# Optimization experiments

Hardware: AMD Instinct MI355X
Metric: run time of the kernel (lower is better)

The kernel has to match this reference:

```python
import jax, jax.numpy as jnp
import numpy as np

VOCAB = 64
EMBED = 256
HIDDEN = 1024
BATCH = 256
SEQLEN = 512


def setup_inputs() -> dict:
    key = jax.random.key(0)
    ks = jax.random.split(key, 5)
    return {
        "x": jax.random.randint(ks[0], (BATCH, SEQLEN), 0, VOCAB),
        "embedding": jax.random.normal(ks[1], (VOCAB, EMBED), dtype=jnp.float32),
        "W_ih": jax.random.normal(ks[2], (EMBED, HIDDEN), dtype=jnp.float32) * 0.01,
        "W_hh": jax.random.normal(ks[3], (HIDDEN, HIDDEN), dtype=jnp.float32) * 0.01,
        "b_h": jnp.zeros((HIDDEN,), dtype=jnp.float32),
        "W_ho": jax.random.normal(ks[4], (HIDDEN, VOCAB), dtype=jnp.float32) * 0.01,
        "b_o": jnp.zeros((VOCAB,), dtype=jnp.float32),
    }


def reference(x, embedding, W_ih, W_hh, b_h, W_ho, b_o):
    # x: [B, L] int indices
    b, l = x.shape
    x_embed = embedding[x]                 # [B, L, E]
    # Precompute the input projection for all timesteps at once: [L, B, H]
    x_proj = jnp.einsum('ble,eh->lbh', x_embed, W_ih) + b_h
    h0 = jnp.zeros((b, W_hh.shape[0]), dtype=x_embed.dtype)

    def step(h_prev, xp_t):
        h_t = jnp.tanh(xp_t + h_prev @ W_hh)   # [B, H]
        return h_t, h_t

    final_hidden, outputs = jax.lax.scan(step, h0, x_proj)  # outputs: [L, B, H]
    outputs = outputs.transpose(1, 0, 2)                    # [B, L, H]
    logits = outputs @ W_ho + b_o                           # [B, L, V]
    return logits, final_hidden
```

## Files before the change

### kernel.cpp

```cpp
#include <hip/hip_runtime.h>
#include <stdint.h>


#define BATCH 256
#define SEQ   512
#define HID   1024
#define VOC   64
#define EMB   256
#define FINAL_OFF (BATCH * SEQ * VOC)
#define RING_SLOTS 32
#define BH (BATCH * HID)
#define CNT_STRIDE 8448

typedef __attribute__((ext_vector_type(8))) short short8;
typedef __attribute__((ext_vector_type(4))) float f32x4;
typedef unsigned long long u64;

__device__ inline unsigned short f2bf(float f) {
  union { float f; unsigned u; } v; v.f = f;
  unsigned u = v.u;
  return (unsigned short)((u + 0x7FFFu + ((u >> 16) & 1u)) >> 16);
}

__device__ __forceinline__ float ftanh(float v) {
  float e = __expf(2.0f * v);
  return fmaf(-2.0f, __builtin_amdgcn_rcpf(e + 1.0f), 1.0f);
}

__device__ inline u64 cload64(const unsigned short* p) {
  return __hip_atomic_load((const u64*)p, __ATOMIC_RELAXED,
                           __HIP_MEMORY_SCOPE_AGENT);
}
__device__ inline void cstore32(unsigned short* p, unsigned v) {
  __hip_atomic_store((unsigned*)p, v, __ATOMIC_RELAXED,
                     __HIP_MEMORY_SCOPE_AGENT);
}

__global__ __launch_bounds__(256) void k_prep(const float* __restrict__ emb,
                                              const float* __restrict__ Wih,
                                              const float* __restrict__ bh,
                                              float* __restrict__ proj) {
  __shared__ float es[EMB];
  const int v = blockIdx.x >> 2;
  const int p = blockIdx.x & 3;
  const int tid = threadIdx.x;
  es[tid] = emb[v * EMB + tid];
  __syncthreads();
  const int h = p * 256 + tid;
  float acc = bh[h];
  for (int e = 0; e < EMB; ++e) acc += es[e] * Wih[e * HID + h];
  proj[v * HID + h] = acc;
}

__global__ __launch_bounds__(256) void k_prep2(const float* __restrict__ Who,
                                               unsigned short* __restrict__ wof) {
  const int e = blockIdx.x * 256 + threadIdx.x;
  const int l15 = e & 15, vt = (e >> 4) & 3, qq = (e >> 6) & 3, kb = e >> 8;
  #pragma unroll
  for (int j = 0; j < 8; ++j)
    wof[e * 8 + j] = f2bf(Who[(kb * 32 + qq * 8 + j) * VOC + vt * 16 + l15]);
}

__global__ __launch_bounds__(256, 1) void k_rnn(
    const int* __restrict__ x, const float* __restrict__ Whh,
    const float* __restrict__ proj, const unsigned short* __restrict__ wof,
    const float* __restrict__ bo, unsigned short* __restrict__ ring,
    float* __restrict__ out, float* __restrict__ final_out,
    unsigned int* __restrict__ cnt) {
  extern __shared__ char smem[];
  unsigned short* w_lds = (unsigned short*)smem;
  char*           h_lds = smem;
  float*          p_lds = (float*)(smem + 33024);
  int*            xs_t  = (int*)(smem + 49664);

  const int tid = threadIdx.x, bid = blockIdx.x;
  const int gi = bid & 15, gj = bid >> 4;
  const int row0 = gi * 16;
  const int lane = tid & 63, wv = tid >> 6;
  const int l15 = lane & 15, q = lane >> 4;

  for (int it = 0; it < 256; ++it) {
    int u = it * 256 + tid;
    int k = u >> 6, n = u & 63;
    int kb = k >> 5, qq = (k >> 3) & 3, j8 = k & 7;
    w_lds[(size_t)kb * 2048 + qq * 512 + n * 8 + j8] =
        f2bf(Whh[k * HID + gj * 64 + n]);
  }
  __syncthreads();

  short8 bfr[32];
  {
    const char* bbase = (const char*)w_lds + q * 1024 + (wv * 16 + l15) * 16;
    #pragma unroll
    for (int kb = 0; kb < 32; ++kb)
      bfr[kb] = *(const short8*)(bbase + (size_t)kb * 4096);
  }
  __syncthreads();

  for (int it = 0; it < 16; ++it) {
    int u = it * 256 + tid;
    int v = u >> 6, c = u & 63;
    p_lds[v * 65 + c] = proj[(size_t)v * HID + gj * 64 + c];
  }
  for (int it = 0; it < 32; ++it) {
    int u = it * 256 + tid;
    int tt = u >> 4, r = u & 15;
    xs_t[tt * 16 + r] = x[(size_t)(row0 + r) * SEQ + tt];
  }
  __syncthreads();

  unsigned int* cnt_i = (unsigned int*)((char*)cnt + gi * CNT_STRIDE);

  const int hcol = gj * 64 + wv * 16 + l15;
  const int pcol = wv * 16 + l15;
  const char* abase = h_lds + l15 * 2064 + q * 16;
  const float bias = bo[wv * 16 + l15];
  const char* wofb = (const char*)wof + ((q * 4 + wv) * 16 + l15) * 16;

  for (int t = 0; t < SEQ; ++t) {
    f32x4 a0 = {0.f, 0.f, 0.f, 0.f}, a1 = {0.f, 0.f, 0.f, 0.f};
    f32x4 a2 = {0.f, 0.f, 0.f, 0.f}, a3 = {0.f, 0.f, 0.f, 0.f};
    if (t > 0) {
      #pragma unroll
      for (int kb = 0; kb < 32; kb += 4) {
        short8 af0 = *(const short8*)(abase + (kb + 0) * 64);
        a0 = __builtin_amdgcn_mfma_f32_16x16x32_bf16(af0, bfr[kb + 0], a0, 0, 0, 0);
        short8 af1 = *(const short8*)(abase + (kb + 1) * 64);
        a1 = __builtin_amdgcn_mfma_f32_16x16x32_bf16(af1, bfr[kb + 1], a1, 0, 0, 0);
        short8 af2 = *(const short8*)(abase + (kb + 2) * 64);
        a2 = __builtin_amdgcn_mfma_f32_16x16x32_bf16(af2, bfr[kb + 2], a2, 0, 0, 0);
        short8 af3 = *(const short8*)(abase + (kb + 3) * 64);
        a3 = __builtin_amdgcn_mfma_f32_16x16x32_bf16(af3, bfr[kb + 3], a3, 0, 0, 0);
      }
    }
    unsigned short* slot = ring + (size_t)(t & (RING_SLOTS - 1)) * BH;
    float hv[4];
    #pragma unroll
    for (int r = 0; r < 4; ++r) {
      int row = q * 4 + r;
      int xi = xs_t[t * 16 + row];
      float av = (a0[r] + a1[r]) + (a2[r] + a3[r]);
      hv[r] = ftanh(p_lds[xi * 65 + pcol] + av);
      if (t == SEQ - 1) final_out[(size_t)(row0 + row) * HID + hcol] = hv[r];
    }
    #pragma unroll
    for (int r = 0; r < 4; ++r) {
      unsigned myb = f2bf(hv[r]);
      unsigned oth = (unsigned)__shfl_xor((int)myb, 1);
      if ((l15 & 1) == 0) {
        int b = row0 + q * 4 + r;
        cstore32(slot + (size_t)b * HID + hcol, myb | (oth << 16));
      }
    }
    __syncthreads();
    if (tid == 0) atomicAdd(cnt_i, 1u);
    if ((t & 15) == 15) {
      int tsel = (t - 16) + gj;
      if (tsel >= 0) {
        const unsigned short* hs =
            ring + (size_t)(tsel & (RING_SLOTS - 1)) * BH +
            (size_t)(row0 + l15) * HID + q * 8;
        f32x4 lc = {0.f, 0.f, 0.f, 0.f};
        for (int g = 0; g < 4; ++g) {
          u64 hb[16];
          #pragma unroll
          for (int j = 0; j < 8; ++j) {
            const unsigned short* pk = hs + (g * 8 + j) * 32;
            hb[2 * j]     = cload64(pk);
            hb[2 * j + 1] = cload64(pk + 4);
          }
          #pragma unroll
          for (int j = 0; j < 8; ++j) {
            union { u64 d[2]; short8 s8; } c;
            c.d[0] = hb[2 * j]; c.d[1] = hb[2 * j + 1];
            short8 w8 = *(const short8*)(wofb + (size_t)(g * 8 + j) * 4096);
            lc = __builtin_amdgcn_mfma_f32_16x16x32_bf16(c.s8, w8, lc, 0, 0, 0);
          }
        }
        #pragma unroll
        for (int rr = 0; rr < 4; ++rr) {
          int b = row0 + q * 4 + rr;
          out[((size_t)b * SEQ + tsel) * VOC + wv * 16 + l15] = lc[rr] + bias;
        }
      }
    }
    if (tid == 0) {
      int guard = 0;
      while (__hip_atomic_load(cnt_i, __ATOMIC_RELAXED,
                               __HIP_MEMORY_SCOPE_AGENT)
             < 16u * (unsigned)(t + 1)) {
        __builtin_amdgcn_s_sleep(1);
        if (++guard > (1 << 16)) break;
      }
    }
    __syncthreads();
    if (t < SEQ - 1) {
      u64 tmp[16];
      #pragma unroll
      for (int rr = 0; rr < 16; ++rr)
        tmp[rr] = cload64(slot + (size_t)(row0 + rr) * HID + tid * 4);
      #pragma unroll
      for (int rr = 0; rr < 16; ++rr)
        *(u64*)(h_lds + rr * 2064 + tid * 8) = tmp[rr];
      __syncthreads();
    }
  }

  if (gj == 15) {
    int tsel = SEQ - 1;
    const unsigned short* hs =
        ring + (size_t)(tsel & (RING_SLOTS - 1)) * BH +
        (size_t)(row0 + l15) * HID + q * 8;
    f32x4 lc = {0.f, 0.f, 0.f, 0.f};
    for (int g = 0; g < 4; ++g) {
      u64 hb[16];
      #pragma unroll
      for (int j = 0; j < 8; ++j) {
        const unsigned short* pk = hs + (g * 8 + j) * 32;
        hb[2 * j]     = cload64(pk);
        hb[2 * j + 1] = cload64(pk + 4);
      }
      #pragma unroll
      for (int j = 0; j < 8; ++j) {
        union { u64 d[2]; short8 s8; } c;
        c.d[0] = hb[2 * j]; c.d[1] = hb[2 * j + 1];
        short8 w8 = *(const short8*)(wofb + (size_t)(g * 8 + j) * 4096);
        lc = __builtin_amdgcn_mfma_f32_16x16x32_bf16(c.s8, w8, lc, 0, 0, 0);
      }
    }
    #pragma unroll
    for (int rr = 0; rr < 4; ++rr) {
      int b = row0 + q * 4 + rr;
      out[((size_t)b * SEQ + tsel) * VOC + wv * 16 + l15] = lc[rr] + bias;
    }
  }
}

extern "C" void kernel_launch(void* const* d_in, const int* in_sizes, int n_in,
                              void* d_out, int out_size, void* d_ws, size_t ws_size,
                              hipStream_t stream) {
  const int*   x   = (const int*)d_in[0];
  const float* emb = (const float*)d_in[1];
  const float* Wih = (const float*)d_in[2];
  const float* Whh = (const float*)d_in[3];
  const float* bh  = (const float*)d_in[4];
  const float* Who = (const float*)d_in[5];
  const float* bo  = (const float*)d_in[6];
  float* out = (float*)d_out;

  char* ws = (char*)d_ws;
  float*          proj = (float*)ws;
  unsigned int*   cnt  = (unsigned int*)(ws + 262144);
  unsigned short* wof  = (unsigned short*)(ws + 524288);
  unsigned short* ring = (unsigned short*)(ws + (1 << 20));

  size_t need = (size_t)(1 << 20) + (size_t)RING_SLOTS * BATCH * HID * 2;
  if (ws_size < need) return;

  (void)hipFuncSetAttribute(reinterpret_cast<const void*>(k_rnn),
                            hipFuncAttributeMaxDynamicSharedMemorySize, 131072);

  k_prep<<<256, 256, 0, stream>>>(emb, Wih, bh, proj);
  k_prep2<<<32, 256, 0, stream>>>(Who, wof);
  hipMemsetAsync(cnt, 0, 262144, stream);
  k_rnn<<<256, 256, 131072, stream>>>(x, Whh, proj, wof, bo, ring,
                                      out, out + FINAL_OFF, cnt);
}
```

Baseline: 1.708 ms.

## Split recurrent matmul over K across waves and shard step counters

Each wave now computes a K-slice (256 of the 1024 hidden inputs) for all four 16-column tiles, sharing one A-fragment load across four MFMAs. The partial sums are then reduced through a new LDS scratch region with an extra barrier per step. This replaces each wave loading all 32 A fragments for its own column tile, so per-wave LDS reads drop by 4x. The single per-group arrival counter is also split into four counters on separate cache lines, polled jointly by four lanes, to reduce atomic contention. The cost is an extra LDS round trip and a __syncthreads on the serial critical path of every timestep.

```diff
diff --git a/kernel.cpp b/kernel.cpp
--- a/kernel.cpp
+++ b/kernel.cpp
@@ -72,6 +72,7 @@
   char*           h_lds = smem;
   float*          p_lds = (float*)(smem + 33024);
   int*            xs_t  = (int*)(smem + 49664);
+  char*           red   = smem + 82432;
 
   const int tid = threadIdx.x, bid = blockIdx.x;
   const int gi = bid & 15, gj = bid >> 4;
@@ -90,10 +91,13 @@
 
   short8 bfr[32];
   {
-    const char* bbase = (const char*)w_lds + q * 1024 + (wv * 16 + l15) * 16;
-    #pragma unroll
-    for (int kb = 0; kb < 32; ++kb)
-      bfr[kb] = *(const short8*)(bbase + (size_t)kb * 4096);
+    const char* bsta = (const char*)w_lds + q * 1024 + l15 * 16;
+    #pragma unroll
+    for (int i = 0; i < 8; ++i)
+      #pragma unroll
+      for (int nt = 0; nt < 4; ++nt)
+        bfr[i * 4 + nt] =
+            *(const short8*)(bsta + (size_t)(wv * 8 + i) * 4096 + nt * 256);
   }
   __syncthreads();
 
@@ -109,7 +113,8 @@
   }
   __syncthreads();
 
-  unsigned int* cnt_i = (unsigned int*)((char*)cnt + gi * CNT_STRIDE);
+  unsigned int* cnt_g = (unsigned int*)((char*)cnt + gi * CNT_STRIDE);
+  unsigned int* cnt_a = cnt_g + (gj & 3) * 32;
 
   const int hcol = gj * 64 + wv * 16 + l15;
   const int pcol = wv * 16 + l15;
@@ -118,20 +123,34 @@
   const char* wofb = (const char*)wof + ((q * 4 + wv) * 16 + l15) * 16;
 
   for (int t = 0; t < SEQ; ++t) {
-    f32x4 a0 = {0.f, 0.f, 0.f, 0.f}, a1 = {0.f, 0.f, 0.f, 0.f};
-    f32x4 a2 = {0.f, 0.f, 0.f, 0.f}, a3 = {0.f, 0.f, 0.f, 0.f};
+    f32x4 p0 = {0.f, 0.f, 0.f, 0.f}, p1 = {0.f, 0.f, 0.f, 0.f};
+    f32x4 p2 = {0.f, 0.f, 0.f, 0.f}, p3 = {0.f, 0.f, 0.f, 0.f};
     if (t > 0) {
       #pragma unroll
-      for (int kb = 0; kb < 32; kb += 4) {
-        short8 af0 = *(const short8*)(abase + (kb + 0) * 64);
-        a0 = __builtin_amdgcn_mfma_f32_16x16x32_bf16(af0, bfr[kb + 0], a0, 0, 0, 0);
-        short8 af1 = *(const short8*)(abase + (kb + 1) * 64);
-        a1 = __builtin_amdgcn_mfma_f32_16x16x32_bf16(af1, bfr[kb + 1], a1, 0, 0, 0);
-        short8 af2 = *(const short8*)(abase + (kb + 2) * 64);
-        a2 = __builtin_amdgcn_mfma_f32_16x16x32_bf16(af2, bfr[kb + 2], a2, 0, 0, 0);
-        short8 af3 = *(const short8*)(abase + (kb + 3) * 64);
-        a3 = __builtin_amdgcn_mfma_f32_16x16x32_bf16(af3, bfr[kb + 3], a3, 0, 0, 0);
-      }
+      for (int i = 0; i < 8; ++i) {
+        short8 af = *(const short8*)(abase + (wv * 8 + i) * 64);
+        p0 = __builtin_amdgcn_mfma_f32_16x16x32_bf16(af, bfr[i * 4 + 0], p0, 0, 0, 0);
+        p1 = __builtin_amdgcn_mfma_f32_16x16x32_bf16(af, bfr[i * 4 + 1], p1, 0, 0, 0);
+        p2 = __builtin_amdgcn_mfma_f32_16x16x32_bf16(af, bfr[i * 4 + 2], p2, 0, 0, 0);
+        p3 = __builtin_amdgcn_mfma_f32_16x16x32_bf16(af, bfr[i * 4 + 3], p3, 0, 0, 0);
+      }
+    }
+    {
+      char* zb = red + ((size_t)(wv * 4) * 64 + lane) * 16;
+      *(f32x4*)(zb)        = p0;
+      *(f32x4*)(zb + 1024) = p1;
+      *(f32x4*)(zb + 2048) = p2;
+      *(f32x4*)(zb + 3072) = p3;
+    }
+    __syncthreads();
+    f32x4 s;
+    {
+      const char* rb = red + ((size_t)wv * 64 + lane) * 16;
+      f32x4 s0 = *(const f32x4*)(rb);
+      f32x4 s1 = *(const f32x4*)(rb + 4096);
+      f32x4 s2 = *(const f32x4*)(rb + 8192);
+      f32x4 s3 = *(const f32x4*)(rb + 12288);
+      s = (s0 + s1) + (s2 + s3);
     }
     unsigned short* slot = ring + (size_t)(t & (RING_SLOTS - 1)) * BH;
     float hv[4];
@@ -139,8 +158,7 @@
     for (int r = 0; r < 4; ++r) {
       int row = q * 4 + r;
       int xi = xs_t[t * 16 + row];
-      float av = (a0[r] + a1[r]) + (a2[r] + a3[r]);
-      hv[r] = ftanh(p_lds[xi * 65 + pcol] + av);
+      hv[r] = ftanh(p_lds[xi * 65 + pcol] + s[r]);
       if (t == SEQ - 1) final_out[(size_t)(row0 + row) * HID + hcol] = hv[r];
     }
     #pragma unroll
@@ -153,7 +171,7 @@
       }
     }
     __syncthreads();
-    if (tid == 0) atomicAdd(cnt_i, 1u);
+    if (tid == 0) atomicAdd(cnt_a, 1u);
     if ((t & 15) == 15) {
       int tsel = (t - 16) + gj;
       if (tsel >= 0) {
@@ -184,13 +202,18 @@
         }
       }
     }
-    if (tid == 0) {
-      int guard = 0;
-      while (__hip_atomic_load(cnt_i, __ATOMIC_RELAXED,
-                               __HIP_MEMORY_SCOPE_AGENT)
-             < 16u * (unsigned)(t + 1)) {
+    if (tid < 64) {
+      const unsigned* cp = cnt_g + tid * 32;
+      int g = 0;
+      for (;;) {
+        int cond = 1;
+        if (tid < 4)
+          cond = (__hip_atomic_load(cp, __ATOMIC_RELAXED,
+                                    __HIP_MEMORY_SCOPE_AGENT)
+                  >= 4u * (unsigned)(t + 1));
+        if (__all(cond)) break;
         __builtin_amdgcn_s_sleep(1);
-        if (++guard > (1 << 16)) break;
+        if (++g > (1 << 16)) break;
       }
     }
     __syncthreads();
```

New measurement: 1.968 ms. 15.2% more time.
